# Kernel optimization log

Hardware: AMD Instinct MI355X
Metric: run time of the kernel (lower is better)

The kernel has to match this reference:

```python
import jax, jax.numpy as jnp
import numpy as np

LN_EPS = 1e-12


def _layernorm(x, gamma, beta):
    mu = jnp.mean(x, axis=-1, keepdims=True)
    var = jnp.mean((x - mu) ** 2, axis=-1, keepdims=True)
    return (x - mu) * jax.lax.rsqrt(var + LN_EPS) * gamma + beta


def _gcn(x, node_emb, time_emb, wpool, bpool, ln_g, ln_b):
    # x: [B,N,C]; node_emb: [N,D]; time_emb: [D]
    e = _layernorm(node_emb + time_emb[None, :], ln_g, ln_b)          # [N,D] (dropout in eval = identity)
    adj = jax.nn.softmax(e @ e.T, axis=1)                             # [N,N] dynamic adjacency
    weights = jnp.einsum('nd,dkio->nkio', e, wpool)                   # [N,2,Cin,Cout] per-node weights
    bias = e @ bpool                                                  # [N,Cout]
    # supports = [I, adj]: identity support is just x itself
    x_g = jnp.stack([x, jnp.einsum('nm,bmc->bnc', adj, x)], axis=2)   # [B,N,2,Cin]
    return jnp.einsum('bnki,nkio->bno', x_g, weights) + bias          # [B,N,Cout]


def setup_inputs() -> dict:
    key = jax.random.key(0)
    ks = jax.random.split(key, 10)
    B, N, Cin, H, D = 32, 2048, 32, 64, 64
    s = 0.1
    return {
        'x': jax.random.normal(ks[0], (B, N, Cin), jnp.float32),
        'state': jax.random.normal(ks[1], (B, N, H), jnp.float32),
        'node_embeddings': jax.random.normal(ks[2], (N, D), jnp.float32),
        'time_embeddings': jax.random.normal(ks[3], (D,), jnp.float32),
        'gate_wpool': jax.random.normal(ks[4], (D, 2, Cin + H, 2 * H), jnp.float32) * s,
        'gate_bpool': jax.random.normal(ks[5], (D, 2 * H), jnp.float32) * s,
        'gate_ln_g': jnp.ones((D,), jnp.float32),
        'gate_ln_b': jnp.zeros((D,), jnp.float32),
        'update_wpool': jax.random.normal(ks[6], (D, 2, Cin + H, H), jnp.float32) * s,
        'update_bpool': jax.random.normal(ks[7], (D, H), jnp.float32) * s,
        'update_ln_g': jnp.ones((D,), jnp.float32),
        'update_ln_b': jnp.zeros((D,), jnp.float32),
    }


def reference(x, state, node_embeddings, time_embeddings,
              gate_wpool, gate_bpool, gate_ln_g, gate_ln_b,
              update_wpool, update_bpool, update_ln_g, update_ln_b):
    H = state.shape[-1]
    inp = jnp.concatenate([x, state], axis=-1)                        # [B,N,Cin+H]
    z_r = jax.nn.sigmoid(_gcn(inp, node_embeddings, time_embeddings,
                              gate_wpool, gate_bpool, gate_ln_g, gate_ln_b))
    z, r = z_r[..., :H], z_r[..., H:]
    cand = jnp.concatenate([x, z * state], axis=-1)
    hc = jnp.tanh(_gcn(cand, node_embeddings, time_embeddings,
                       update_wpool, update_bpool, update_ln_g, update_ln_b))
    return r * state + (1.0 - r) * hc
```

## Files before the change

### kernel.cpp

```cpp
#include <hip/hip_runtime.h>

typedef _Float16 f16;
typedef _Float16 half8 __attribute__((ext_vector_type(8)));
typedef float f32x4 __attribute__((ext_vector_type(4)));

#define NN 2048
#define BB 32
#define CINC 32
#define HH 64
#define DD 64
#define C1 96
#define KI 192
#define OG 128
#define OU 64
#define WCG 24576
#define WCU 12288

#define XGI(n, ks, b, kk) \
  ((((((size_t)(n)) * 6 + (ks)) * 4 + ((kk) >> 3)) * BB + (b)) * 8 + ((kk) & 7))

__device__ __forceinline__ f32x4 mfma16(half8 a, half8 b, f32x4 c) {
  return __builtin_amdgcn_mfma_f32_16x16x32_f16(a, b, c, 0, 0, 0);
}

typedef __attribute__((address_space(1))) const void* gas_t;
typedef __attribute__((address_space(3))) void* las_t;
__device__ __forceinline__ void gl_lds16(const void* g, void* l) {
  __builtin_amdgcn_global_load_lds((gas_t)g, (las_t)l, 16, 0, 0);
}

#define SWZ(row, kb) (((row) << 7) + ((kb) ^ (((row) & 7) << 4)))

__global__ __launch_bounds__(256) void k_ln_bias(
    const float* __restrict__ ne, const float* __restrict__ te,
    const float* __restrict__ gg, const float* __restrict__ gb,
    const float* __restrict__ ug, const float* __restrict__ ub,
    const float* __restrict__ gbp, const float* __restrict__ ubp,
    f16* __restrict__ egh, f16* __restrict__ euh,
    float* __restrict__ biasg, float* __restrict__ biasu) {
  __shared__ float esg[4][64];
  __shared__ float esu[4][64];
  int nl = threadIdx.x >> 6;
  int node = blockIdx.x * 4 + nl;
  int d = threadIdx.x & 63;
  float v = ne[node * DD + d] + te[d];
  float s = v;
  #pragma unroll
  for (int m = 1; m < 64; m <<= 1) s += __shfl_xor(s, m, 64);
  float mu = s * (1.f / 64.f);
  float df = v - mu;
  float q = df * df;
  #pragma unroll
  for (int m = 1; m < 64; m <<= 1) q += __shfl_xor(q, m, 64);
  float rs = rsqrtf(q * (1.f / 64.f) + 1e-12f);
  float base = df * rs;
  float a = base * gg[d] + gb[d];
  float b = base * ug[d] + ub[d];
  egh[node * DD + d] = (f16)a;
  euh[node * DD + d] = (f16)b;
  esg[nl][d] = a; esu[nl][d] = b;
  __syncthreads();
  #pragma unroll
  for (int i = 0; i < 3; ++i) {
    int u = i * 256 + threadIdx.x;
    int un = u / 192, oo = u % 192;
    int n2 = blockIdx.x * 4 + un;
    float acc = 0.f;
    if (oo < OG) {
      #pragma unroll 8
      for (int dd = 0; dd < 64; ++dd) acc += esg[un][dd] * gbp[dd * OG + oo];
      biasg[(size_t)n2 * OG + oo] = acc;
    } else {
      int o = oo - OG;
      #pragma unroll 8
      for (int dd = 0; dd < 64; ++dd) acc += esu[un][dd] * ubp[dd * OU + o];
      biasu[(size_t)n2 * OU + o] = acc;
    }
  }
}

__global__ __launch_bounds__(256) void k_wpool_t(const float* __restrict__ gwp,
                                                 const float* __restrict__ uwp,
                                                 f16* __restrict__ wtg,
                                                 f16* __restrict__ wtu) {
  const int upd = blockIdx.z;
  if (upd && blockIdx.y >= OU / 16) return;
  const float* wpool = upd ? uwp : gwp;
  f16* wt = upd ? wtu : wtg;
  const int O = upd ? OU : OG;
  __shared__ float tile[64][17];
  int ki = blockIdx.x;
  int o0 = blockIdx.y * 16;
  int t = threadIdx.x;
  const int seg = (ki >> 5) * 4 + ((ki >> 3) & 3);
  const int kkl = ki & 7;
  #pragma unroll
  for (int i = 0; i < 4; ++i) {
    int e2 = i * 256 + t;
    int d = e2 >> 4, o = e2 & 15;
    tile[d][o] = wpool[((size_t)d * KI + ki) * O + o0 + o];
  }
  __syncthreads();
  #pragma unroll
  for (int i = 0; i < 4; ++i) {
    int e2 = i * 256 + t;
    int o = e2 >> 6, d = e2 & 63;
    size_t row = ((size_t)seg * O + (o0 + o)) * 8 + kkl;
    wt[row * DD + d] = (f16)tile[d][o];
  }
}

__global__ __launch_bounds__(256) void k_build_inp(const float* __restrict__ x,
                                                   const float* __restrict__ st,
                                                   f16* __restrict__ cm,
                                                   f16* __restrict__ xg,
                                                   f16* __restrict__ sth) {
  __shared__ f16 tile[96][66];
  int mb = blockIdx.x * 64;
  int b = blockIdx.y;
  int t = threadIdx.x;
  #pragma unroll
  for (int i = 0; i < 24; ++i) {
    int e2 = i * 256 + t;
    int m = e2 / 96, c = e2 % 96;
    float v = (c < CINC) ? x[((size_t)b * NN + mb + m) * CINC + c]
                         : st[((size_t)b * NN + mb + m) * HH + c - CINC];
    f16 h = (f16)v;
    tile[c][m] = h;
    xg[XGI(mb + m, c >> 5, b, c & 31)] = h;
    if (c >= CINC) sth[((size_t)b * NN + mb + m) * HH + c - CINC] = h;
  }
  __syncthreads();
  #pragma unroll
  for (int i = 0; i < 24; ++i) {
    int e2 = i * 256 + t;
    int c = e2 >> 6, m = e2 & 63;
    cm[((size_t)b * C1 + c) * NN + mb + m] = tile[c][m];
  }
}

__global__ __launch_bounds__(256) void k_transpose_zs(const f16* __restrict__ zs,
                                                      f16* __restrict__ cm) {
  __shared__ f16 tile[64][66];
  int mb = blockIdx.x * 64;
  int b = blockIdx.y;
  int t = threadIdx.x;
  #pragma unroll
  for (int i = 0; i < 16; ++i) {
    int e2 = i * 256 + t;
    int m = e2 >> 6, o = e2 & 63;
    tile[o][m] = zs[((size_t)b * NN + mb + m) * HH + o];
  }
  __syncthreads();
  #pragma unroll
  for (int i = 0; i < 16; ++i) {
    int e2 = i * 256 + t;
    int o = e2 >> 6, m = e2 & 63;
    cm[((size_t)b * C1 + CINC + o) * NN + mb + m] = tile[o][m];
  }
}

__global__ __launch_bounds__(256) void k_attn(const f16* __restrict__ eh,
                                              f16* __restrict__ adj) {
  const int r0 = blockIdx.x * 16;
  const int w = threadIdx.x >> 6, lane = threadIdx.x & 63;
  const int fr = lane & 15, fq = lane >> 4;
  __shared__ float pm[4][16], ps[4][16];
  __shared__ float fm[16], fs[16];
  const half8 a0 = *(const half8*)&eh[(size_t)(r0 + fr) * DD + fq * 8];
  const half8 a1 = *(const half8*)&eh[(size_t)(r0 + fr) * DD + 32 + fq * 8];
  float m[4], s[4];
  #pragma unroll
  for (int r = 0; r < 4; ++r) { m[r] = -3.0e38f; s[r] = 0.f; }
  for (int ct = 0; ct < 32; ++ct) {
    const int c0 = w * 512 + ct * 16;
    half8 b0 = *(const half8*)&eh[(size_t)(c0 + fr) * DD + fq * 8];
    half8 b1 = *(const half8*)&eh[(size_t)(c0 + fr) * DD + 32 + fq * 8];
    f32x4 d = mfma16(a0, b0, f32x4{0.f, 0.f, 0.f, 0.f});
    d = mfma16(a1, b1, d);
    #pragma unroll
    for (int r = 0; r < 4; ++r) {
      float mn = fmaxf(m[r], d[r]);
      s[r] = s[r] * __expf(m[r] - mn) + __expf(d[r] - mn);
      m[r] = mn;
    }
  }
  #pragma unroll
  for (int r = 0; r < 4; ++r) {
    #pragma unroll
    for (int mk = 1; mk < 16; mk <<= 1) {
      float mo = __shfl_xor(m[r], mk, 64);
      float so = __shfl_xor(s[r], mk, 64);
      float mn = fmaxf(m[r], mo);
      s[r] = s[r] * __expf(m[r] - mn) + so * __expf(mo - mn);
      m[r] = mn;
    }
  }
  if (fr == 0) {
    #pragma unroll
    for (int r = 0; r < 4; ++r) { pm[w][fq * 4 + r] = m[r]; ps[w][fq * 4 + r] = s[r]; }
  }
  __syncthreads();
  if (threadIdx.x < 16) {
    float M = -3.0e38f;
    #pragma unroll
    for (int i = 0; i < 4; ++i) M = fmaxf(M, pm[i][threadIdx.x]);
    float S = 0.f;
    #pragma unroll
    for (int i = 0; i < 4; ++i) S += ps[i][threadIdx.x] * __expf(pm[i][threadIdx.x] - M);
    fm[threadIdx.x] = M; fs[threadIdx.x] = 1.f / S;
  }
  __syncthreads();
  float Mr[4], Sr[4];
  #pragma unroll
  for (int r = 0; r < 4; ++r) { Mr[r] = fm[fq * 4 + r]; Sr[r] = fs[fq * 4 + r]; }
  for (int ct = 0; ct < 32; ++ct) {
    const int c0 = w * 512 + ct * 16;
    half8 b0 = *(const half8*)&eh[(size_t)(c0 + fr) * DD + fq * 8];
    half8 b1 = *(const half8*)&eh[(size_t)(c0 + fr) * DD + 32 + fq * 8];
    f32x4 d = mfma16(a0, b0, f32x4{0.f, 0.f, 0.f, 0.f});
    d = mfma16(a1, b1, d);
    #pragma unroll
    for (int r = 0; r < 4; ++r)
      adj[(size_t)(r0 + fq * 4 + r) * NN + c0 + fr] = (f16)(__expf(d[r] - Mr[r]) * Sr[r]);
  }
}

#define BM 64
#define BN 96

__global__ __launch_bounds__(256, 4) void k_gemm_xa(const f16* __restrict__ A,
                                                    const f16* __restrict__ Bm,
                                                    f16* __restrict__ xg) {
  const int orig = blockIdx.x;
  const int xcd = orig & 7, j = orig >> 3;
  const int nb = (j >> 2) * BM;
  const int by = (xcd << 2) + (j & 3);
  const int cb = by * BN;
  const int tid = threadIdx.x;
  const int w = tid >> 6, lane = tid & 63;
  const int wr = (w >> 1) * 32, wc = (w & 1) * 48;
  const int fr = lane & 15, fq = lane >> 4;

  const int arow = tid >> 3;
  const int acolb = ((tid & 7) * 16) ^ ((arow & 7) << 4);
  const char* asrc = (const char*)A + (size_t)(nb + arow) * (NN * 2) + acolb;
  const char* bsrc = (const char*)Bm + (size_t)(cb + arow) * (NN * 2) + acolb;

  __shared__ f16 Al[2][BM * 64];
  __shared__ f16 Bl[2][BN * 64];
  auto stage = [&](int buf, int kt) {
    const size_t ko = (size_t)kt * 2;
    char* ad = (char*)&Al[buf][0] + (w << 10);
    char* bd = (char*)&Bl[buf][0] + (w << 10);
    gl_lds16(asrc + ko, ad);
    gl_lds16(asrc + ko + (size_t)32 * (NN * 2), ad + 4096);
    gl_lds16(bsrc + ko, bd);
    gl_lds16(bsrc + ko + (size_t)32 * (NN * 2), bd + 4096);
    gl_lds16(bsrc + ko + (size_t)64 * (NN * 2), bd + 8192);
  };

  f32x4 acc[2][3] = {};
  stage(0, 0);
  for (int kt = 0; kt < NN; kt += 64) {
    const int cur = (kt >> 6) & 1;
    if (kt + 64 < NN) {
      stage(cur ^ 1, kt + 64);
      asm volatile("s_waitcnt vmcnt(5)" ::: "memory");
    } else {
      asm volatile("s_waitcnt vmcnt(0)" ::: "memory");
    }
    __builtin_amdgcn_sched_barrier(0);
    __builtin_amdgcn_s_barrier();
    const char* Ab = (const char*)&Al[cur][0];
    const char* Bb = (const char*)&Bl[cur][0];
    half8 af[2][2], bf[2][3];
    #pragma unroll
    for (int k0 = 0; k0 < 2; ++k0) {
      const int kb = k0 * 64 + fq * 16;
      #pragma unroll
      for (int mt = 0; mt < 2; ++mt)
        af[k0][mt] = *(const half8*)(Ab + SWZ(wr + mt * 16 + fr, kb));
      #pragma unroll
      for (int nt = 0; nt < 3; ++nt)
        bf[k0][nt] = *(const half8*)(Bb + SWZ(wc + nt * 16 + fr, kb));
    }
    asm volatile("s_waitcnt lgkmcnt(0)" ::: "memory");
    __builtin_amdgcn_sched_barrier(0);
    __builtin_amdgcn_s_barrier();
    #pragma unroll
    for (int k0 = 0; k0 < 2; ++k0)
      #pragma unroll
      for (int mt = 0; mt < 2; ++mt)
        #pragma unroll
        for (int nt = 0; nt < 3; ++nt)
          acc[mt][nt] = mfma16(af[k0][mt], bf[k0][nt], acc[mt][nt]);
  }
  #pragma unroll
  for (int mt = 0; mt < 2; ++mt)
    #pragma unroll
    for (int nt = 0; nt < 3; ++nt)
      #pragma unroll
      for (int r = 0; r < 4; ++r) {
        int n = nb + wr + mt * 16 + fq * 4 + r;
        int l = wc + nt * 16 + fr;
        xg[XGI(n, 3 + (l >> 5), by, l & 31)] = (f16)acc[mt][nt][r];
      }
}

__global__ __launch_bounds__(256) void k_gemm_w2(const f16* __restrict__ A,
                                                 const f16* __restrict__ B,
                                                 f16* __restrict__ W, int ncols) {
  __shared__ f16 Al[128 * 64];
  __shared__ f16 Bl[128 * 64];
  const int cb = blockIdx.x * 128;
  const int nb = blockIdx.y * 128;
  const int tid = threadIdx.x;
  const int w = tid >> 6, lane = tid & 63;
  const int wr = (w >> 1) * 64, wc = (w & 1) * 64;
  const int fr = lane & 15, fq = lane >> 4;
  const int arow = tid >> 3;
  const int acolb = ((tid & 7) * 16) ^ ((arow & 7) << 4);
  const char* asrc = (const char*)A + (size_t)(nb + arow) * 128 + acolb;
  const char* bsrc = (const char*)B + (size_t)(cb + arow) * 128 + acolb;
  char* ad = (char*)Al + (w << 10);
  char* bd = (char*)Bl + (w << 10);
  #pragma unroll
  for (int j = 0; j < 4; ++j) gl_lds16(asrc + (size_t)j * 32 * 128, ad + j * 4096);
  #pragma unroll
  for (int j = 0; j < 4; ++j) gl_lds16(bsrc + (size_t)j * 32 * 128, bd + j * 4096);
  __syncthreads();
  f32x4 acc[4][4] = {};
  #pragma unroll
  for (int k0 = 0; k0 < 2; ++k0) {
    const int kb = k0 * 64 + fq * 16;
    half8 af[4], bf[4];
    #pragma unroll
    for (int mt = 0; mt < 4; ++mt)
      af[mt] = *(const half8*)((const char*)Al + SWZ(wr + mt * 16 + fr, kb));
    #pragma unroll
    for (int nt = 0; nt < 4; ++nt)
      bf[nt] = *(const half8*)((const char*)Bl + SWZ(wc + nt * 16 + fr, kb));
    #pragma unroll
    for (int mt = 0; mt < 4; ++mt)
      #pragma unroll
      for (int nt = 0; nt < 4; ++nt)
        acc[mt][nt] = mfma16(af[mt], bf[nt], acc[mt][nt]);
  }
  #pragma unroll
  for (int mt = 0; mt < 4; ++mt)
    #pragma unroll
    for (int nt = 0; nt < 4; ++nt)
      #pragma unroll
      for (int r = 0; r < 4; ++r) {
        int n = nb + wr + mt * 16 + fq * 4 + r;
        int c = cb + wc + nt * 16 + fr;
        W[(size_t)n * ncols + c] = (f16)acc[mt][nt][r];
      }
}

template <bool GATE>
__global__ __launch_bounds__(256, GATE ? 2 : 4) void k_apply4(
    const f16* __restrict__ xg, const f16* __restrict__ W,
    const float* __restrict__ bias,
    const f16* __restrict__ sth,
    f16* xgw, f16* __restrict__ zs, f16* __restrict__ rbuf,
    float* __restrict__ outp) {
  constexpr int O = GATE ? OG : OU;
  constexpr int WB = O * KI * 2;
  constexpr int XB = KI * BB * 2;
  constexpr int NOT_ = GATE ? 2 : 1;
  __shared__ __align__(128) char lds[WB + XB];
  const int n = blockIdx.x;
  const int tid = threadIdx.x;
  const int w = tid >> 6, lane = tid & 63;
  const int fr = lane & 15, fq = lane >> 4;

  const char* wsrc = (const char*)W + (size_t)n * WB + tid * 16;
  const char* xsrc = (const char*)xg + (size_t)n * XB + tid * 16;
  char* wdst = lds + (w << 10);
  char* xdst = lds + WB + (w << 10);
  #pragma unroll
  for (int j = 0; j < WB / 4096; ++j) gl_lds16(wsrc + j * 4096, wdst + j * 4096);
  #pragma unroll
  for (int j = 0; j < XB / 4096; ++j) gl_lds16(xsrc + j * 4096, xdst + j * 4096);
  __syncthreads();

  const char* xl = lds + WB;
  f32x4 acc[2][NOT_] = {};
  #pragma unroll
  for (int ks = 0; ks < 6; ++ks) {
    const int seg = (ks * 4 + fq);
    half8 af0 = *(const half8*)(xl + (seg * 32 + fr) * 16);
    half8 af1 = *(const half8*)(xl + (seg * 32 + 16 + fr) * 16);
    #pragma unroll
    for (int ot = 0; ot < NOT_; ++ot) {
      const int o = (GATE ? (w * 2 + ot) : w) * 16 + fr;
      half8 bf = *(const half8*)(lds + (seg * O + o) * 16);
      acc[0][ot] = mfma16(af0, bf, acc[0][ot]);
      acc[1][ot] = mfma16(af1, bf, acc[1][ot]);
    }
  }
  #pragma unroll
  for (int mt = 0; mt < 2; ++mt)
    #pragma unroll
    for (int ot = 0; ot < NOT_; ++ot) {
      const int o = (GATE ? (w * 2 + ot) : w) * 16 + fr;
      const float bs = bias[(size_t)n * O + o];
      #pragma unroll
      for (int r = 0; r < 4; ++r) {
        int b = mt * 16 + fq * 4 + r;
        float val = acc[mt][ot][r] + bs;
        if (GATE) {
          float s = 1.f / (1.f + expf(-val));
          if (o < HH) {
            size_t bno = ((size_t)b * NN + n) * HH + o;
            float zst = s * (float)sth[bno];
            xgw[XGI(n, 1 + (o >> 5), b, o & 31)] = (f16)zst;
            zs[bno] = (f16)zst;
          } else {
            rbuf[((size_t)b * NN + n) * HH + (o - HH)] = (f16)s;
          }
        } else {
          size_t bno = ((size_t)b * NN + n) * HH + o;
          float hc = tanhf(val);
          float rr = (float)rbuf[bno];
          outp[bno] = rr * (float)sth[bno] + (1.f - rr) * hc;
        }
      }
    }
}

extern "C" void kernel_launch(void* const* d_in, const int* in_sizes, int n_in,
                              void* d_out, int out_size, void* d_ws, size_t ws_size,
                              hipStream_t stream) {
  const float* x   = (const float*)d_in[0];
  const float* st  = (const float*)d_in[1];
  const float* ne  = (const float*)d_in[2];
  const float* te  = (const float*)d_in[3];
  const float* gwp = (const float*)d_in[4];
  const float* gbp = (const float*)d_in[5];
  const float* gg  = (const float*)d_in[6];
  const float* gb  = (const float*)d_in[7];
  const float* uwp = (const float*)d_in[8];
  const float* ubp = (const float*)d_in[9];
  const float* ug  = (const float*)d_in[10];
  const float* ub  = (const float*)d_in[11];
  float* out = (float*)d_out;

  char* wsb = (char*)d_ws;
  size_t off = 0;
  auto alloc = [&](size_t bytes) {
    char* p = wsb + off;
    off = (off + bytes + 255) & ~(size_t)255;
    return p;
  };
  f16*   egh   = (f16*)  alloc((size_t)NN * DD * 2);
  f16*   euh   = (f16*)  alloc((size_t)NN * DD * 2);
  float* biasg = (float*)alloc((size_t)NN * OG * 4);
  float* biasu = (float*)alloc((size_t)NN * OU * 4);
  f16*   wtg   = (f16*)  alloc((size_t)WCG * DD * 2);
  f16*   wtu   = (f16*)  alloc((size_t)WCU * DD * 2);
  f16*   xg    = (f16*)  alloc((size_t)NN * BB * KI * 2);
  f16*   cm    = (f16*)  alloc((size_t)BB * C1 * NN * 2);
  f16*   zs    = (f16*)  alloc((size_t)BB * NN * HH * 2);
  f16*   rbuf  = (f16*)  alloc((size_t)BB * NN * HH * 2);
  f16*   sth   = (f16*)  alloc((size_t)BB * NN * HH * 2);
  f16*   adj   = (f16*)  alloc((size_t)NN * NN * 2);
  f16*   W     = (f16*)  alloc((size_t)NN * WCG * 2);
  (void)ws_size; (void)in_sizes; (void)n_in; (void)out_size;

  hipLaunchKernelGGL(k_ln_bias, dim3(NN / 4), dim3(256), 0, stream,
                     ne, te, gg, gb, ug, ub, gbp, ubp,
                     egh, euh, biasg, biasu);
  hipLaunchKernelGGL(k_wpool_t, dim3(KI, OG / 16, 2), dim3(256), 0, stream,
                     gwp, uwp, wtg, wtu);
  hipLaunchKernelGGL(k_build_inp, dim3(NN / 64, BB), dim3(256), 0, stream,
                     x, st, cm, xg, sth);

  hipLaunchKernelGGL(k_attn, dim3(NN / 16), dim3(256), 0, stream, egh, adj);
  hipLaunchKernelGGL(k_gemm_xa, dim3(1024), dim3(256), 0, stream, adj, cm, xg);
  hipLaunchKernelGGL(k_gemm_w2, dim3(WCG / 128, NN / 128), dim3(256), 0, stream,
                     egh, wtg, W, WCG);
  hipLaunchKernelGGL((k_apply4<true>), dim3(NN), dim3(256), 0, stream,
                     xg, W, biasg, sth, xg, zs, rbuf, (float*)nullptr);
  hipLaunchKernelGGL(k_transpose_zs, dim3(NN / 64, BB), dim3(256), 0, stream, zs, cm);

  hipLaunchKernelGGL(k_attn, dim3(NN / 16), dim3(256), 0, stream, euh, adj);
  hipLaunchKernelGGL(k_gemm_xa, dim3(1024), dim3(256), 0, stream, adj, cm, xg);
  hipLaunchKernelGGL(k_gemm_w2, dim3(WCU / 128, NN / 128), dim3(256), 0, stream,
                     euh, wtu, W, WCU);
  hipLaunchKernelGGL((k_apply4<false>), dim3(NN), dim3(256), 0, stream,
                     xg, W, biasu, sth, (f16*)nullptr, (f16*)nullptr, rbuf, out);
}
```

Baseline: 239.5 us.

## Double-buffer per-node weight chunks in apply kernel to overlap loads with MFMA

The apply kernel previously loaded the whole per-node weight matrix (48KB for the gate) plus the input tile into LDS before computing. It now streams the weights in six K-chunks through a two-buffer LDS ring, prefetching the next chunk while computing on the current one with explicit vmcnt waits and barriers. This shrinks LDS use, allowing 4 blocks per CU for the gate kernel too, and is meant to hide global load latency. In exchange it adds barriers and hand-counted waitcnts per chunk, which may stall or serialize given the tiny amount of compute per chunk.

```diff
diff --git a/kernel.cpp b/kernel.cpp
--- a/kernel.cpp
+++ b/kernel.cpp
@@ -360,45 +360,66 @@
 }
 
 template <bool GATE>
-__global__ __launch_bounds__(256, GATE ? 2 : 4) void k_apply4(
+__global__ __launch_bounds__(256, 4) void k_apply6(
     const f16* __restrict__ xg, const f16* __restrict__ W,
     const float* __restrict__ bias,
     const f16* __restrict__ sth,
     f16* xgw, f16* __restrict__ zs, f16* __restrict__ rbuf,
     float* __restrict__ outp) {
   constexpr int O = GATE ? OG : OU;
-  constexpr int WB = O * KI * 2;
-  constexpr int XB = KI * BB * 2;
+  constexpr int WS = GATE ? WCG : WCU;
+  constexpr int CHB = O * 64;
+  constexpr int CHL = CHB / 4096;
+  constexpr int XB = 12288;
   constexpr int NOT_ = GATE ? 2 : 1;
-  __shared__ __align__(128) char lds[WB + XB];
+  __shared__ __align__(128) char Wl[2][CHB];
+  __shared__ __align__(128) char Xl[XB];
   const int n = blockIdx.x;
   const int tid = threadIdx.x;
   const int w = tid >> 6, lane = tid & 63;
   const int fr = lane & 15, fq = lane >> 4;
 
-  const char* wsrc = (const char*)W + (size_t)n * WB + tid * 16;
+  const char* wbase = (const char*)W + (size_t)n * (WS * 2);
   const char* xsrc = (const char*)xg + (size_t)n * XB + tid * 16;
-  char* wdst = lds + (w << 10);
-  char* xdst = lds + WB + (w << 10);
-  #pragma unroll
-  for (int j = 0; j < WB / 4096; ++j) gl_lds16(wsrc + j * 4096, wdst + j * 4096);
+  char* xdst = Xl + (w << 10);
   #pragma unroll
   for (int j = 0; j < XB / 4096; ++j) gl_lds16(xsrc + j * 4096, xdst + j * 4096);
-  __syncthreads();
-
-  const char* xl = lds + WB;
+  auto stageW = [&](int buf, int ks) {
+    const char* src = wbase + ks * CHB + tid * 16;
+    char* dst = Wl[buf] + (w << 10);
+    #pragma unroll
+    for (int j = 0; j < CHL; ++j) gl_lds16(src + j * 4096, dst + j * 4096);
+  };
+
   f32x4 acc[2][NOT_] = {};
+  stageW(0, 0);
   #pragma unroll
   for (int ks = 0; ks < 6; ++ks) {
-    const int seg = (ks * 4 + fq);
-    half8 af0 = *(const half8*)(xl + (seg * 32 + fr) * 16);
-    half8 af1 = *(const half8*)(xl + (seg * 32 + 16 + fr) * 16);
+    const int cur = ks & 1;
+    if (ks < 5) {
+      stageW(cur ^ 1, ks + 1);
+      if constexpr (GATE) asm volatile("s_waitcnt vmcnt(2)" ::: "memory");
+      else                asm volatile("s_waitcnt vmcnt(1)" ::: "memory");
+    } else {
+      asm volatile("s_waitcnt vmcnt(0)" ::: "memory");
+    }
+    __builtin_amdgcn_sched_barrier(0);
+    __builtin_amdgcn_s_barrier();
+    half8 af0 = *(const half8*)(Xl + ((ks * 4 + fq) * 32 + fr) * 16);
+    half8 af1 = *(const half8*)(Xl + ((ks * 4 + fq) * 32 + 16 + fr) * 16);
+    half8 bf[NOT_];
     #pragma unroll
     for (int ot = 0; ot < NOT_; ++ot) {
       const int o = (GATE ? (w * 2 + ot) : w) * 16 + fr;
-      half8 bf = *(const half8*)(lds + (seg * O + o) * 16);
-      acc[0][ot] = mfma16(af0, bf, acc[0][ot]);
-      acc[1][ot] = mfma16(af1, bf, acc[1][ot]);
+      bf[ot] = *(const half8*)(Wl[cur] + (fq * O + o) * 16);
+    }
+    asm volatile("s_waitcnt lgkmcnt(0)" ::: "memory");
+    __builtin_amdgcn_sched_barrier(0);
+    __builtin_amdgcn_s_barrier();
+    #pragma unroll
+    for (int ot = 0; ot < NOT_; ++ot) {
+      acc[0][ot] = mfma16(af0, bf[ot], acc[0][ot]);
+      acc[1][ot] = mfma16(af1, bf[ot], acc[1][ot]);
     }
   }
   #pragma unroll
@@ -482,7 +503,7 @@
   hipLaunchKernelGGL(k_gemm_xa, dim3(1024), dim3(256), 0, stream, adj, cm, xg);
   hipLaunchKernelGGL(k_gemm_w2, dim3(WCG / 128, NN / 128), dim3(256), 0, stream,
                      egh, wtg, W, WCG);
-  hipLaunchKernelGGL((k_apply4<true>), dim3(NN), dim3(256), 0, stream,
+  hipLaunchKernelGGL((k_apply6<true>), dim3(NN), dim3(256), 0, stream,
                      xg, W, biasg, sth, xg, zs, rbuf, (float*)nullptr);
   hipLaunchKernelGGL(k_transpose_zs, dim3(NN / 64, BB), dim3(256), 0, stream, zs, cm);
 
@@ -490,6 +511,6 @@
   hipLaunchKernelGGL(k_gemm_xa, dim3(1024), dim3(256), 0, stream, adj, cm, xg);
   hipLaunchKernelGGL(k_gemm_w2, dim3(WCU / 128, NN / 128), dim3(256), 0, stream,
                      euh, wtu, W, WCU);
-  hipLaunchKernelGGL((k_apply4<false>), dim3(NN), dim3(256), 0, stream,
+  hipLaunchKernelGGL((k_apply6<false>), dim3(NN), dim3(256), 0, stream,
                      xg, W, biasu, sth, (f16*)nullptr, (f16*)nullptr, rbuf, out);
 }
```

After: 226.8 us. 5.3% less time.

## Fuse per-node weight generation into apply kernel and batch both attention passes

Applied to the files above, without the earlier changes.

Drops the global per-node weight matrix W (NN x 24576 f16) and its separate GEMM. Each apply block now computes its 16 nodes' weights on the fly from the embeddings and the re-laid-out wpool into swizzled LDS, then applies them to the graph-convolved inputs. Both adjacency softmax computations run in one launch, and a second xg buffer lets the gate and update stages avoid overwriting each other. This removes a large write and read of W through HBM, at the cost of recomputing weights per block, lower occupancy (launch bounds 1) and an extra adjacency buffer.

```diff
diff --git a/kernel.cpp b/kernel.cpp
--- a/kernel.cpp
+++ b/kernel.cpp
@@ -2,6 +2,7 @@
 
 typedef _Float16 f16;
 typedef _Float16 half8 __attribute__((ext_vector_type(8)));
+typedef _Float16 half4 __attribute__((ext_vector_type(4)));
 typedef float f32x4 __attribute__((ext_vector_type(4)));
 
 #define NN 2048
@@ -13,8 +14,6 @@
 #define KI 192
 #define OG 128
 #define OU 64
-#define WCG 24576
-#define WCU 12288
 
 #define XGI(n, ks, b, kk) \
   ((((((size_t)(n)) * 6 + (ks)) * 4 + ((kk) >> 3)) * BB + (b)) * 8 + ((kk) & 7))
@@ -92,8 +91,6 @@
   int ki = blockIdx.x;
   int o0 = blockIdx.y * 16;
   int t = threadIdx.x;
-  const int seg = (ki >> 5) * 4 + ((ki >> 3) & 3);
-  const int kkl = ki & 7;
   #pragma unroll
   for (int i = 0; i < 4; ++i) {
     int e2 = i * 256 + t;
@@ -105,7 +102,9 @@
   for (int i = 0; i < 4; ++i) {
     int e2 = i * 256 + t;
     int o = e2 >> 6, d = e2 & 63;
-    size_t row = ((size_t)seg * O + (o0 + o)) * 8 + kkl;
+    const int og = o0 + o;
+    size_t row = (((size_t)(og >> 6) * 6 + (ki >> 5)) * 128 +
+                  ((og & 63) * 2 + ((ki >> 4) & 1))) * 16 + (ki & 15);
     wt[row * DD + d] = (f16)tile[d][o];
   }
 }
@@ -114,6 +113,7 @@
                                                    const float* __restrict__ st,
                                                    f16* __restrict__ cm,
                                                    f16* __restrict__ xg,
+                                                   f16* __restrict__ xg2,
                                                    f16* __restrict__ sth) {
   __shared__ f16 tile[96][66];
   int mb = blockIdx.x * 64;
@@ -128,7 +128,8 @@
     f16 h = (f16)v;
     tile[c][m] = h;
     xg[XGI(mb + m, c >> 5, b, c & 31)] = h;
-    if (c >= CINC) sth[((size_t)b * NN + mb + m) * HH + c - CINC] = h;
+    if (c < CINC) xg2[XGI(mb + m, 0, b, c)] = h;
+    else sth[((size_t)b * NN + mb + m) * HH + c - CINC] = h;
   }
   __syncthreads();
   #pragma unroll
@@ -160,8 +161,12 @@
   }
 }
 
-__global__ __launch_bounds__(256) void k_attn(const f16* __restrict__ eh,
-                                              f16* __restrict__ adj) {
+__global__ __launch_bounds__(256) void k_attn(const f16* __restrict__ eg,
+                                              const f16* __restrict__ eu,
+                                              f16* __restrict__ adjg,
+                                              f16* __restrict__ adju) {
+  const f16* eh = blockIdx.y ? eu : eg;
+  f16* adj = blockIdx.y ? adju : adjg;
   const int r0 = blockIdx.x * 16;
   const int w = threadIdx.x >> 6, lane = threadIdx.x & 63;
   const int fr = lane & 15, fq = lane >> 4;
@@ -308,127 +313,119 @@
       }
 }
 
-__global__ __launch_bounds__(256) void k_gemm_w2(const f16* __restrict__ A,
-                                                 const f16* __restrict__ B,
-                                                 f16* __restrict__ W, int ncols) {
-  __shared__ f16 Al[128 * 64];
-  __shared__ f16 Bl[128 * 64];
-  const int cb = blockIdx.x * 128;
-  const int nb = blockIdx.y * 128;
-  const int tid = threadIdx.x;
-  const int w = tid >> 6, lane = tid & 63;
-  const int wr = (w >> 1) * 64, wc = (w & 1) * 64;
-  const int fr = lane & 15, fq = lane >> 4;
-  const int arow = tid >> 3;
-  const int acolb = ((tid & 7) * 16) ^ ((arow & 7) << 4);
-  const char* asrc = (const char*)A + (size_t)(nb + arow) * 128 + acolb;
-  const char* bsrc = (const char*)B + (size_t)(cb + arow) * 128 + acolb;
-  char* ad = (char*)Al + (w << 10);
-  char* bd = (char*)Bl + (w << 10);
-  #pragma unroll
-  for (int j = 0; j < 4; ++j) gl_lds16(asrc + (size_t)j * 32 * 128, ad + j * 4096);
-  #pragma unroll
-  for (int j = 0; j < 4; ++j) gl_lds16(bsrc + (size_t)j * 32 * 128, bd + j * 4096);
-  __syncthreads();
-  f32x4 acc[4][4] = {};
-  #pragma unroll
-  for (int k0 = 0; k0 < 2; ++k0) {
-    const int kb = k0 * 64 + fq * 16;
-    half8 af[4], bf[4];
-    #pragma unroll
-    for (int mt = 0; mt < 4; ++mt)
-      af[mt] = *(const half8*)((const char*)Al + SWZ(wr + mt * 16 + fr, kb));
-    #pragma unroll
-    for (int nt = 0; nt < 4; ++nt)
-      bf[nt] = *(const half8*)((const char*)Bl + SWZ(wc + nt * 16 + fr, kb));
-    #pragma unroll
-    for (int mt = 0; mt < 4; ++mt)
-      #pragma unroll
-      for (int nt = 0; nt < 4; ++nt)
-        acc[mt][nt] = mfma16(af[mt], bf[nt], acc[mt][nt]);
-  }
-  #pragma unroll
-  for (int mt = 0; mt < 4; ++mt)
-    #pragma unroll
-    for (int nt = 0; nt < 4; ++nt)
-      #pragma unroll
-      for (int r = 0; r < 4; ++r) {
-        int n = nb + wr + mt * 16 + fq * 4 + r;
-        int c = cb + wc + nt * 16 + fr;
-        W[(size_t)n * ncols + c] = (f16)acc[mt][nt][r];
-      }
-}
-
 template <bool GATE>
-__global__ __launch_bounds__(256, GATE ? 2 : 4) void k_apply4(
-    const f16* __restrict__ xg, const f16* __restrict__ W,
+__global__ __launch_bounds__(256, 1) void k_wap(
+    const f16* __restrict__ eh, const f16* __restrict__ wt2,
+    const f16* __restrict__ xgr,
     const float* __restrict__ bias,
     const f16* __restrict__ sth,
-    f16* xgw, f16* __restrict__ zs, f16* __restrict__ rbuf,
+    f16* __restrict__ xg2, f16* __restrict__ zs, f16* __restrict__ rbuf,
     float* __restrict__ outp) {
-  constexpr int O = GATE ? OG : OU;
-  constexpr int WB = O * KI * 2;
-  constexpr int XB = KI * BB * 2;
-  constexpr int NOT_ = GATE ? 2 : 1;
-  __shared__ __align__(128) char lds[WB + XB];
-  const int n = blockIdx.x;
+  __shared__ __align__(128) char Wc[16 * 4096];
+  const int nodebase = blockIdx.x * 16;
+  const int half = GATE ? blockIdx.y : 0;
   const int tid = threadIdx.x;
   const int w = tid >> 6, lane = tid & 63;
   const int fr = lane & 15, fq = lane >> 4;
 
-  const char* wsrc = (const char*)W + (size_t)n * WB + tid * 16;
-  const char* xsrc = (const char*)xg + (size_t)n * XB + tid * 16;
-  char* wdst = lds + (w << 10);
-  char* xdst = lds + WB + (w << 10);
-  #pragma unroll
-  for (int j = 0; j < WB / 4096; ++j) gl_lds16(wsrc + j * 4096, wdst + j * 4096);
-  #pragma unroll
-  for (int j = 0; j < XB / 4096; ++j) gl_lds16(xsrc + j * 4096, xdst + j * 4096);
-  __syncthreads();
-
-  const char* xl = lds + WB;
-  f32x4 acc[2][NOT_] = {};
-  #pragma unroll
+  const half8 e0 = *(const half8*)&eh[(size_t)(nodebase + fr) * DD + fq * 8];
+  const half8 e1 = *(const half8*)&eh[(size_t)(nodebase + fr) * DD + 32 + fq * 8];
+
+  const char* wbase = (const char*)wt2 + (size_t)half * 6 * 128 * 2048;
+
+  f32x4 acc[4][2][4] = {};
+
   for (int ks = 0; ks < 6; ++ks) {
-    const int seg = (ks * 4 + fq);
-    half8 af0 = *(const half8*)(xl + (seg * 32 + fr) * 16);
-    half8 af1 = *(const half8*)(xl + (seg * 32 + 16 + fr) * 16);
-    #pragma unroll
-    for (int ot = 0; ot < NOT_; ++ot) {
-      const int o = (GATE ? (w * 2 + ot) : w) * 16 + fr;
-      half8 bf = *(const half8*)(lds + (seg * O + o) * 16);
-      acc[0][ot] = mfma16(af0, bf, acc[0][ot]);
-      acc[1][ot] = mfma16(af1, bf, acc[1][ot]);
-    }
-  }
-  #pragma unroll
-  for (int mt = 0; mt < 2; ++mt)
-    #pragma unroll
-    for (int ot = 0; ot < NOT_; ++ot) {
-      const int o = (GATE ? (w * 2 + ot) : w) * 16 + fr;
-      const float bs = bias[(size_t)n * O + o];
-      #pragma unroll
-      for (int r = 0; r < 4; ++r) {
-        int b = mt * 16 + fq * 4 + r;
-        float val = acc[mt][ot][r] + bs;
-        if (GATE) {
-          float s = 1.f / (1.f + expf(-val));
-          if (o < HH) {
-            size_t bno = ((size_t)b * NN + n) * HH + o;
-            float zst = s * (float)sth[bno];
-            xgw[XGI(n, 1 + (o >> 5), b, o & 31)] = (f16)zst;
-            zs[bno] = (f16)zst;
-          } else {
-            rbuf[((size_t)b * NN + n) * HH + (o - HH)] = (f16)s;
-          }
-        } else {
-          size_t bno = ((size_t)b * NN + n) * HH + o;
-          float hc = tanhf(val);
-          float rr = (float)rbuf[bno];
-          outp[bno] = rr * (float)sth[bno] + (1.f - rr) * hc;
+    const char* cbase = wbase + (size_t)ks * 128 * 2048 + fr * 128 + fq * 16;
+    half8 sa[2][8][2];
+    #pragma unroll
+    for (int j = 0; j < 8; ++j) {
+      const char* p = cbase + (size_t)(w * 32 + j) * 2048;
+      sa[0][j][0] = *(const half8*)p;
+      sa[0][j][1] = *(const half8*)(p + 64);
+    }
+    #pragma unroll
+    for (int g = 0; g < 4; ++g) {
+      const int cur = g & 1;
+      if (g < 3) {
+        #pragma unroll
+        for (int j = 0; j < 8; ++j) {
+          const char* p = cbase + (size_t)(w * 32 + (g + 1) * 8 + j) * 2048;
+          sa[cur ^ 1][j][0] = *(const half8*)p;
+          sa[cur ^ 1][j][1] = *(const half8*)(p + 64);
         }
       }
-    }
+      __builtin_amdgcn_sched_barrier(0);
+      #pragma unroll
+      for (int j = 0; j < 8; ++j) {
+        const int T = w * 32 + g * 8 + j;
+        const int o_local = T >> 1, khalf = T & 1;
+        f32x4 d = mfma16(sa[cur][j][0], e0, f32x4{0.f, 0.f, 0.f, 0.f});
+        d = mfma16(sa[cur][j][1], e1, d);
+        half4 h4;
+        #pragma unroll
+        for (int r = 0; r < 4; ++r) h4[r] = (f16)d[r];
+        int a = (fr << 12) + o_local * 64 + khalf * 32 + fq * 8;
+        a ^= (((fr ^ o_local) & 7) << 4);
+        *(half4*)(Wc + a) = h4;
+      }
+    }
+    __syncthreads();
+    half8 af[4][2];
+    #pragma unroll
+    for (int j2 = 0; j2 < 4; ++j2) {
+      const int n = nodebase + w * 4 + j2;
+      af[j2][0] = *(const half8*)&xgr[XGI(n, ks, fr, fq * 8)];
+      af[j2][1] = *(const half8*)&xgr[XGI(n, ks, 16 + fr, fq * 8)];
+    }
+    __builtin_amdgcn_sched_barrier(0);
+    #pragma unroll
+    for (int j2 = 0; j2 < 4; ++j2) {
+      const int nd = w * 4 + j2;
+      #pragma unroll
+      for (int ot = 0; ot < 4; ++ot) {
+        const int ol = ot * 16 + fr;
+        int a = (nd << 12) + ol * 64 + fq * 16;
+        a ^= (((nd ^ ol) & 7) << 4);
+        half8 bf = *(const half8*)(Wc + a);
+        acc[j2][0][ot] = mfma16(af[j2][0], bf, acc[j2][0][ot]);
+        acc[j2][1][ot] = mfma16(af[j2][1], bf, acc[j2][1][ot]);
+      }
+    }
+    __syncthreads();
+  }
+  #pragma unroll
+  for (int j2 = 0; j2 < 4; ++j2) {
+    const int n = nodebase + w * 4 + j2;
+    #pragma unroll
+    for (int ot = 0; ot < 4; ++ot) {
+      const int o = half * 64 + ot * 16 + fr;
+      const float bs = bias[(size_t)n * (GATE ? OG : OU) + o];
+      #pragma unroll
+      for (int mt = 0; mt < 2; ++mt)
+        #pragma unroll
+        for (int r = 0; r < 4; ++r) {
+          const int b = mt * 16 + fq * 4 + r;
+          const float val = acc[j2][mt][ot][r] + bs;
+          if (GATE) {
+            const float s = 1.f / (1.f + expf(-val));
+            if (half == 0) {
+              const size_t bno = ((size_t)b * NN + n) * HH + o;
+              const float zst = s * (float)sth[bno];
+              xg2[XGI(n, 1 + (o >> 5), b, o & 31)] = (f16)zst;
+              zs[bno] = (f16)zst;
+            } else {
+              rbuf[((size_t)b * NN + n) * HH + (o - HH)] = (f16)s;
+            }
+          } else {
+            const size_t bno = ((size_t)b * NN + n) * HH + o;
+            const float hc = tanhf(val);
+            const float rr = (float)rbuf[bno];
+            outp[bno] = rr * (float)sth[bno] + (1.f - rr) * hc;
+          }
+        }
+    }
+  }
 }
 
 extern "C" void kernel_launch(void* const* d_in, const int* in_sizes, int n_in,
@@ -459,15 +456,16 @@
   f16*   euh   = (f16*)  alloc((size_t)NN * DD * 2);
   float* biasg = (float*)alloc((size_t)NN * OG * 4);
   float* biasu = (float*)alloc((size_t)NN * OU * 4);
-  f16*   wtg   = (f16*)  alloc((size_t)WCG * DD * 2);
-  f16*   wtu   = (f16*)  alloc((size_t)WCU * DD * 2);
+  f16*   wtg   = (f16*)  alloc((size_t)OG * KI * DD * 2);
+  f16*   wtu   = (f16*)  alloc((size_t)OU * KI * DD * 2);
   f16*   xg    = (f16*)  alloc((size_t)NN * BB * KI * 2);
+  f16*   xg2   = (f16*)  alloc((size_t)NN * BB * KI * 2);
   f16*   cm    = (f16*)  alloc((size_t)BB * C1 * NN * 2);
   f16*   zs    = (f16*)  alloc((size_t)BB * NN * HH * 2);
   f16*   rbuf  = (f16*)  alloc((size_t)BB * NN * HH * 2);
   f16*   sth   = (f16*)  alloc((size_t)BB * NN * HH * 2);
   f16*   adj   = (f16*)  alloc((size_t)NN * NN * 2);
-  f16*   W     = (f16*)  alloc((size_t)NN * WCG * 2);
+  f16*   adju  = (f16*)  alloc((size_t)NN * NN * 2);
   (void)ws_size; (void)in_sizes; (void)n_in; (void)out_size;
 
   hipLaunchKernelGGL(k_ln_bias, dim3(NN / 4), dim3(256), 0, stream,
@@ -476,20 +474,16 @@
   hipLaunchKernelGGL(k_wpool_t, dim3(KI, OG / 16, 2), dim3(256), 0, stream,
                      gwp, uwp, wtg, wtu);
   hipLaunchKernelGGL(k_build_inp, dim3(NN / 64, BB), dim3(256), 0, stream,
-                     x, st, cm, xg, sth);
-
-  hipLaunchKernelGGL(k_attn, dim3(NN / 16), dim3(256), 0, stream, egh, adj);
+                     x, st, cm, xg, xg2, sth);
+  hipLaunchKernelGGL(k_attn, dim3(NN / 16, 2), dim3(256), 0, stream,
+                     egh, euh, adj, adju);
+
   hipLaunchKernelGGL(k_gemm_xa, dim3(1024), dim3(256), 0, stream, adj, cm, xg);
-  hipLaunchKernelGGL(k_gemm_w2, dim3(WCG / 128, NN / 128), dim3(256), 0, stream,
-                     egh, wtg, W, WCG);
-  hipLaunchKernelGGL((k_apply4<true>), dim3(NN), dim3(256), 0, stream,
-                     xg, W, biasg, sth, xg, zs, rbuf, (float*)nullptr);
+  hipLaunchKernelGGL((k_wap<true>), dim3(NN / 16, 2), dim3(256), 0, stream,
+                     egh, wtg, xg, biasg, sth, xg2, zs, rbuf, (float*)nullptr);
   hipLaunchKernelGGL(k_transpose_zs, dim3(NN / 64, BB), dim3(256), 0, stream, zs, cm);
 
-  hipLaunchKernelGGL(k_attn, dim3(NN / 16), dim3(256), 0, stream, euh, adj);
-  hipLaunchKernelGGL(k_gemm_xa, dim3(1024), dim3(256), 0, stream, adj, cm, xg);
-  hipLaunchKernelGGL(k_gemm_w2, dim3(WCU / 128, NN / 128), dim3(256), 0, stream,
-                     euh, wtu, W, WCU);
-  hipLaunchKernelGGL((k_apply4<false>), dim3(NN), dim3(256), 0, stream,
-                     xg, W, biasu, sth, (f16*)nullptr, (f16*)nullptr, rbuf, out);
-}
+  hipLaunchKernelGGL(k_gemm_xa, dim3(1024), dim3(256), 0, stream, adju, cm, xg2);
+  hipLaunchKernelGGL((k_wap<false>), dim3(NN / 16, 1), dim3(256), 0, stream,
+                     euh, wtu, xg2, biasu, sth, (f16*)nullptr, (f16*)nullptr, rbuf, out);
+}
```

Result: slower. 372.5 us (+55.5%).
